# Kernel optimization log

Measured on AMD Instinct MI355X. Metric: run time of the kernel, lower is better.

The kernel has to match this reference:

```python
import jax, jax.numpy as jnp
import numpy as np


def _bag_mean(idx, table):
    # F.embedding_bag(mode='mean', padding_idx=last row): padding entries are
    # excluded from both the sum and the count. idx: [B, S, K]
    pad = table.shape[0] - 1
    mask = (idx != pad)[..., None].astype(table.dtype)          # [B,S,K,1]
    emb = table[idx] * mask                                      # [B,S,K,D]
    cnt = mask.sum(axis=-2)                                      # [B,S,1]
    s = emb.sum(axis=-2)                                         # [B,S,D]
    return jnp.where(cnt > 0, s / jnp.maximum(cnt, 1.0), 0.0)


def _subgraph_parts(qq, ques_table, skill_table, diff_table, area_table,
                    ques2skill, ques2diff, ques2area):
    qe = ques_table[qq]                                          # [B,S,D]
    sk = _bag_mean(ques2skill[qq], skill_table)                  # [B,S,D]
    df = diff_table[ques2diff[qq][..., 0]]                       # [B,S,D]
    ar = area_table[ques2area[qq][..., 0]]                       # [B,S,D]
    return qe, sk, df, ar


def reference(q, a, next_q, ques_table, skill_table, diff_table, area_table,
              ques2skill, ques2diff, ques2area, Wq, bq):
    # ---- get_subgraph_embedding (non-JunYi path) ----
    qe, sk, df, ar = _subgraph_parts(q, ques_table, skill_table, diff_table,
                                     area_table, ques2skill, ques2diff, ques2area)
    q_emb = (qe + sk + df + ar) / 4.0

    nqe, nsk, ndf, nar = _subgraph_parts(next_q, ques_table, skill_table,
                                         diff_table, area_table, ques2skill,
                                         ques2diff, ques2area)
    nq_emb = (nqe + nsk + ndf + nar) / 4.0
    # faithful to source: the averaging line for next_q is applied twice
    nq_emb = (nq_emb + nsk + ndf + nar) / 4.0

    q_emb = q_emb @ Wq.T + bq
    nq_emb = nq_emb @ Wq.T + bq

    # ---- Fusion_Module: answer==1 keeps first half, answer==0 keeps second ----
    af = a[..., None].astype(q_emb.dtype)                        # [B,S,1]
    input_emb = jnp.concatenate([q_emb * af, q_emb * (1.0 - af)], axis=-1)

    return jnp.concatenate([input_emb, nq_emb], axis=-1)        # [B,S,3D]


def setup_inputs() -> dict:
    key = jax.random.key(0)
    ks = jax.random.split(key, 12)
    B, S, D = 16, 2048, 128
    NQ, NS, ND, NA, K = 200001, 2001, 100, 50, 8
    return {
        "q": jax.random.randint(ks[0], (B, S), 0, NQ - 1),
        "a": jax.random.randint(ks[1], (B, S), 0, 2),
        "next_q": jax.random.randint(ks[2], (B, S), 0, NQ - 1),
        "ques_table": jax.random.normal(ks[3], (NQ, D), jnp.float32),
        "skill_table": jax.random.normal(ks[4], (NS, D), jnp.float32),
        "diff_table": jax.random.normal(ks[5], (ND, D), jnp.float32),
        "area_table": jax.random.normal(ks[6], (NA, D), jnp.float32),
        "ques2skill": jax.random.randint(ks[7], (NQ, K), 0, NS),
        "ques2diff": jax.random.randint(ks[8], (NQ, 1), 0, ND),
        "ques2area": jax.random.randint(ks[9], (NQ, 1), 0, NA),
        "Wq": jax.random.normal(ks[10], (D, D), jnp.float32) / np.sqrt(D),
        "bq": jax.random.normal(ks[11], (D,), jnp.float32) * 0.01,
    }
```

## Files before the change

### kernel.cpp

```cpp
#include <hip/hip_runtime.h>
#include <hip/hip_bf16.h>

typedef float  f32x4  __attribute__((ext_vector_type(4)));
typedef short  s16x8  __attribute__((ext_vector_type(8)));

#define PIN_LOADS() asm volatile("" ::: "memory")

__device__ __forceinline__ unsigned short f2bf(float f) {
    unsigned int u = __float_as_uint(f);
    unsigned int rnd = 0x7fffu + ((u >> 16) & 1u);
    return (unsigned short)((u + rnd) >> 16);
}

__device__ __forceinline__ void bf8_fma(const s16x8 v, float s, f32x4& a0, f32x4& a1) {
    const uint4 u = *(const uint4*)&v;
    a0[0] += s * __uint_as_float(u.x << 16);
    a0[1] += s * __uint_as_float(u.x & 0xffff0000u);
    a0[2] += s * __uint_as_float(u.y << 16);
    a0[3] += s * __uint_as_float(u.y & 0xffff0000u);
    a1[0] += s * __uint_as_float(u.z << 16);
    a1[1] += s * __uint_as_float(u.z & 0xffff0000u);
    a1[2] += s * __uint_as_float(u.w << 16);
    a1[3] += s * __uint_as_float(u.w & 0xffff0000u);
}

__global__ __launch_bounds__(256)
void h2kt_prep_wqb(const float* __restrict__ Wq, unsigned short* __restrict__ Wqb) {
    const int s  = blockIdx.x * 256 + threadIdx.x;
    const int f  = s >> 6, sl = s & 63;
    const int jt = f >> 2, kt = f & 3;
    const int row = jt * 16 + (sl & 15);
    const int col = kt * 32 + (sl >> 4) * 8;
    const float4 w0 = *(const float4*)(Wq + row * 128 + col);
    const float4 w1 = *(const float4*)(Wq + row * 128 + col + 4);
    s16x8 v;
    v[0] = (short)f2bf(w0.x); v[1] = (short)f2bf(w0.y);
    v[2] = (short)f2bf(w0.z); v[3] = (short)f2bf(w0.w);
    v[4] = (short)f2bf(w1.x); v[5] = (short)f2bf(w1.y);
    v[6] = (short)f2bf(w1.z); v[7] = (short)f2bf(w1.w);
    *(s16x8*)(Wqb + (size_t)s * 8) = v;
}

__global__ __launch_bounds__(64)
void h2kt_prep_tables(const float* __restrict__ skill, const float* __restrict__ diff,
                      const float* __restrict__ area, const unsigned short* __restrict__ Wqb,
                      unsigned short* __restrict__ T2)
{
    const int lane = threadIdx.x;
    const int cl = lane & 15, grp = lane >> 4;
    const int row16 = blockIdx.x * 16;

    int srow = row16 + cl;
    if (srow > 2150) srow = 2150;
    const float* src = (srow < 2001) ? skill + (size_t)srow * 128
                     : (srow < 2101) ? diff + (size_t)(srow - 2001) * 128
                                     : area + (size_t)(srow - 2101) * 128;
    s16x8 afr[4];
    #pragma unroll
    for (int kt = 0; kt < 4; ++kt) {
        const float4 v0 = *(const float4*)(src + kt * 32 + grp * 8);
        const float4 v1 = *(const float4*)(src + kt * 32 + grp * 8 + 4);
        s16x8 v;
        v[0] = (short)f2bf(v0.x); v[1] = (short)f2bf(v0.y);
        v[2] = (short)f2bf(v0.z); v[3] = (short)f2bf(v0.w);
        v[4] = (short)f2bf(v1.x); v[5] = (short)f2bf(v1.y);
        v[6] = (short)f2bf(v1.z); v[7] = (short)f2bf(v1.w);
        afr[kt] = v;
    }
    #pragma unroll
    for (int jt = 0; jt < 8; ++jt) {
        f32x4 acc = {0.f, 0.f, 0.f, 0.f};
        #pragma unroll
        for (int kt = 0; kt < 4; ++kt) {
            const s16x8 bf = *(const s16x8*)(Wqb + ((size_t)(jt * 4 + kt) * 64 + lane) * 8);
            acc = __builtin_amdgcn_mfma_f32_16x16x32_bf16(afr[kt], bf, acc, 0, 0, 0);
        }
        #pragma unroll
        for (int r = 0; r < 4; ++r) {
            const int orow = row16 + grp * 4 + r;
            if (orow < 2151) T2[(size_t)orow * 128 + jt * 16 + cl] = f2bf(acc[r]);
        }
    }
}

__global__ __launch_bounds__(128, 4)
void h2kt_fused(const int* __restrict__ q, const int* __restrict__ a_arr,
                const int* __restrict__ next_q,
                const float* __restrict__ ques_table,
                const int* __restrict__ q2s,
                const int* __restrict__ q2d,
                const int* __restrict__ q2a,
                const unsigned short* __restrict__ T2,
                const unsigned short* __restrict__ Wqb,
                const float* __restrict__ bq,
                float* __restrict__ out,
                int pad_idx)
{
    __shared__ __align__(16) unsigned char U[16 * 132 * 4];
    unsigned short* Q = (unsigned short*)U;
    float*          D = (float*)U;

    const int tid  = threadIdx.x;
    const int w    = tid >> 6;
    const int lane = tid & 63;
    const int cl   = lane & 15;
    const int grp  = lane >> 4;
    const int r0   = blockIdx.x * 16;
    const int base = r0 & 32767;
    const bool isnq = (r0 >= 32768);
    const int* __restrict__ QQ = isnq ? next_q : q;
    const float wq_ = isnq ? 0.0625f : 0.25f;
    const float wr_ = isnq ? 0.3125f : 0.25f;

    const int r2 = lane >> 5;
    const int c  = lane & 31;
    int qqv[4];
    #pragma unroll
    for (int p = 0; p < 4; ++p) qqv[p] = QQ[base + w * 8 + p * 2 + r2];

    const int row0 = w * 8 + grp;
    const int row1 = w * 8 + 4 + grp;
    const int qq20 = QQ[base + row0];
    const int qq21 = QQ[base + row1];
    int av0 = 1, av1 = 1;
    if (!isnq) { av0 = a_arr[base + row0]; av1 = a_arr[base + row1]; }

    f32x4 qv[4];
    #pragma unroll
    for (int p = 0; p < 4; ++p)
        qv[p] = *(const f32x4*)(ques_table + (size_t)qqv[p] * 128 + c * 4);

    const int4 A03 = *(const int4*)(q2s + (size_t)qq20 * 8);
    const int4 A47 = *(const int4*)(q2s + (size_t)qq20 * 8 + 4);
    const int4 B03 = *(const int4*)(q2s + (size_t)qq21 * 8);
    const int4 B47 = *(const int4*)(q2s + (size_t)qq21 * 8 + 4);
    const int di0 = q2d[qq20], ai0 = q2a[qq20];
    const int di1 = q2d[qq21], ai1 = q2a[qq21];
    const int sa[8] = {A03.x, A03.y, A03.z, A03.w, A47.x, A47.y, A47.z, A47.w};
    const int sb[8] = {B03.x, B03.y, B03.z, B03.w, B47.x, B47.y, B47.z, B47.w};

    s16x8 t0[10];
    #pragma unroll
    for (int i = 0; i < 8; ++i)
        t0[i] = *(const s16x8*)(T2 + (size_t)sa[i] * 128 + cl * 8);
    t0[8] = *(const s16x8*)(T2 + (size_t)(2001 + di0) * 128 + cl * 8);
    t0[9] = *(const s16x8*)(T2 + (size_t)(2101 + ai0) * 128 + cl * 8);
    PIN_LOADS();

    #pragma unroll
    for (int p = 0; p < 4; ++p) {
        ushort4 o;
        o.x = f2bf(wq_ * qv[p][0]); o.y = f2bf(wq_ * qv[p][1]);
        o.z = f2bf(wq_ * qv[p][2]); o.w = f2bf(wq_ * qv[p][3]);
        *(ushort4*)(Q + (size_t)(w * 8 + p * 2 + r2) * 136 + c * 4) = o;
    }

    s16x8 t1[10];
    #pragma unroll
    for (int i = 0; i < 8; ++i)
        t1[i] = *(const s16x8*)(T2 + (size_t)sb[i] * 128 + cl * 8);
    t1[8] = *(const s16x8*)(T2 + (size_t)(2001 + di1) * 128 + cl * 8);
    t1[9] = *(const s16x8*)(T2 + (size_t)(2101 + ai1) * 128 + cl * 8);
    PIN_LOADS();

    int cnt0 = 0, cnt1 = 0;
    #pragma unroll
    for (int i = 0; i < 8; ++i) { cnt0 += (sa[i] != pad_idx); cnt1 += (sb[i] != pad_idx); }
    const float cs0 = cnt0 > 0 ? wr_ / (float)cnt0 : 0.f;
    const float cs1 = cnt1 > 0 ? wr_ / (float)cnt1 : 0.f;

    f32x4 restA[2], restB[2];
    {
        f32x4 a0 = {0.f,0.f,0.f,0.f}, a1 = {0.f,0.f,0.f,0.f};
        #pragma unroll
        for (int i = 0; i < 8; ++i) bf8_fma(t0[i], (sa[i] != pad_idx) ? cs0 : 0.f, a0, a1);
        bf8_fma(t0[8], wr_, a0, a1);
        bf8_fma(t0[9], wr_, a0, a1);
        restA[0] = a0; restB[0] = a1;
    }
    {
        f32x4 a0 = {0.f,0.f,0.f,0.f}, a1 = {0.f,0.f,0.f,0.f};
        #pragma unroll
        for (int i = 0; i < 8; ++i) bf8_fma(t1[i], (sb[i] != pad_idx) ? cs1 : 0.f, a0, a1);
        bf8_fma(t1[8], wr_, a0, a1);
        bf8_fma(t1[9], wr_, a0, a1);
        restA[1] = a0; restB[1] = a1;
    }

    __syncthreads();

    s16x8 afr[4];
    #pragma unroll
    for (int kt = 0; kt < 4; ++kt)
        afr[kt] = *(const s16x8*)(Q + (size_t)cl * 136 + kt * 32 + grp * 8);

    __syncthreads();

    #pragma unroll
    for (int jt2 = 0; jt2 < 4; ++jt2) {
        const int jt = w * 4 + jt2;
        f32x4 acc = {0.f, 0.f, 0.f, 0.f};
        #pragma unroll
        for (int kt = 0; kt < 4; ++kt) {
            const s16x8 bf = *(const s16x8*)(Wqb + ((size_t)(jt * 4 + kt) * 64 + lane) * 8);
            acc = __builtin_amdgcn_mfma_f32_16x16x32_bf16(afr[kt], bf, acc, 0, 0, 0);
        }
        #pragma unroll
        for (int r = 0; r < 4; ++r)
            D[(size_t)(grp * 4 + r) * 132 + jt * 16 + cl] = acc[r];
    }

    __syncthreads();

    const f32x4 bq0 = *(const f32x4*)(bq + cl * 8);
    const f32x4 bq1 = *(const f32x4*)(bq + cl * 8 + 4);
    const f32x4 z = {0.f, 0.f, 0.f, 0.f};
    #pragma unroll
    for (int p = 0; p < 2; ++p) {
        const int row = w * 8 + p * 4 + grp;
        const f32x4 d0 = *(const f32x4*)(D + (size_t)row * 132 + cl * 8);
        const f32x4 d1 = *(const f32x4*)(D + (size_t)row * 132 + cl * 8 + 4);
        const f32x4 v0 = d0 + restA[p] + bq0;
        const f32x4 v1 = d1 + restB[p] + bq1;
        const size_t orow = (size_t)(base + row);
        const int avv = (p == 0) ? av0 : av1;
        if (!isnq) {
            const bool on = (avv != 0);
            *(f32x4*)(out + orow * 384 + cl * 8)           = on ? v0 : z;
            *(f32x4*)(out + orow * 384 + cl * 8 + 4)       = on ? v1 : z;
            *(f32x4*)(out + orow * 384 + 128 + cl * 8)     = on ? z : v0;
            *(f32x4*)(out + orow * 384 + 128 + cl * 8 + 4) = on ? z : v1;
        } else {
            *(f32x4*)(out + orow * 384 + 256 + cl * 8)     = v0;
            *(f32x4*)(out + orow * 384 + 256 + cl * 8 + 4) = v1;
        }
    }
}

extern "C" void kernel_launch(void* const* d_in, const int* in_sizes, int n_in,
                              void* d_out, int out_size, void* d_ws, size_t ws_size,
                              hipStream_t stream) {
    const int*   q          = (const int*)d_in[0];
    const int*   a          = (const int*)d_in[1];
    const int*   next_q     = (const int*)d_in[2];
    const float* ques_table = (const float*)d_in[3];
    const float* skill_tab  = (const float*)d_in[4];
    const float* diff_tab   = (const float*)d_in[5];
    const float* area_tab   = (const float*)d_in[6];
    const int*   q2s        = (const int*)d_in[7];
    const int*   q2d        = (const int*)d_in[8];
    const int*   q2a        = (const int*)d_in[9];
    const float* Wq         = (const float*)d_in[10];
    const float* bq         = (const float*)d_in[11];
    float* out = (float*)d_out;

    const int NS = in_sizes[4] / 128;
    const int pad_idx = NS - 1;

    unsigned short* Wqb = (unsigned short*)d_ws;
    unsigned short* T2  = Wqb + (size_t)2048 * 8;

    h2kt_prep_wqb<<<8, 256, 0, stream>>>(Wq, Wqb);
    h2kt_prep_tables<<<135, 64, 0, stream>>>(skill_tab, diff_tab, area_tab, Wqb, T2);
    h2kt_fused<<<4096, 128, 0, stream>>>(q, a, next_q, ques_table,
                                         q2s, q2d, q2a, T2, Wqb, bq, out, pad_idx);
}
```

Baseline: 44.78 us.

## Merge prep kernels and precompute per-row gather descriptors before fused kernel

The two prep kernels become one launch. Blocks in that launch now do three jobs: convert Wq to bf16, project the skill/diff/area tables (reading Wq directly instead of waiting on Wqb), and build a 48-byte descriptor per row holding the question id, skill ids, diff/area row offsets and the answer bit. The fused kernel then reads these descriptors instead of chasing q -> q2s/q2d/q2a itself. This removes one launch and a dependent gather stage from the main kernel. In exchange it adds about 3 MB of descriptor writes and reads through the workspace.

```diff
diff --git a/kernel.cpp b/kernel.cpp
--- a/kernel.cpp
+++ b/kernel.cpp
@@ -25,71 +25,98 @@
 }
 
 __global__ __launch_bounds__(256)
-void h2kt_prep_wqb(const float* __restrict__ Wq, unsigned short* __restrict__ Wqb) {
-    const int s  = blockIdx.x * 256 + threadIdx.x;
-    const int f  = s >> 6, sl = s & 63;
-    const int jt = f >> 2, kt = f & 3;
-    const int row = jt * 16 + (sl & 15);
-    const int col = kt * 32 + (sl >> 4) * 8;
-    const float4 w0 = *(const float4*)(Wq + row * 128 + col);
-    const float4 w1 = *(const float4*)(Wq + row * 128 + col + 4);
-    s16x8 v;
-    v[0] = (short)f2bf(w0.x); v[1] = (short)f2bf(w0.y);
-    v[2] = (short)f2bf(w0.z); v[3] = (short)f2bf(w0.w);
-    v[4] = (short)f2bf(w1.x); v[5] = (short)f2bf(w1.y);
-    v[6] = (short)f2bf(w1.z); v[7] = (short)f2bf(w1.w);
-    *(s16x8*)(Wqb + (size_t)s * 8) = v;
-}
-
-__global__ __launch_bounds__(64)
-void h2kt_prep_tables(const float* __restrict__ skill, const float* __restrict__ diff,
-                      const float* __restrict__ area, const unsigned short* __restrict__ Wqb,
-                      unsigned short* __restrict__ T2)
+void h2kt_prep(const float* __restrict__ Wq,
+               const float* __restrict__ skill, const float* __restrict__ diff,
+               const float* __restrict__ area,
+               const int* __restrict__ q, const int* __restrict__ next_q,
+               const int* __restrict__ a_arr,
+               const int* __restrict__ q2s, const int* __restrict__ q2d,
+               const int* __restrict__ q2a,
+               unsigned short* __restrict__ Wqb,
+               unsigned short* __restrict__ T2,
+               int* __restrict__ desc,
+               int pad_idx)
 {
-    const int lane = threadIdx.x;
-    const int cl = lane & 15, grp = lane >> 4;
-    const int row16 = blockIdx.x * 16;
-
-    int srow = row16 + cl;
-    if (srow > 2150) srow = 2150;
-    const float* src = (srow < 2001) ? skill + (size_t)srow * 128
-                     : (srow < 2101) ? diff + (size_t)(srow - 2001) * 128
-                                     : area + (size_t)(srow - 2101) * 128;
-    s16x8 afr[4];
-    #pragma unroll
-    for (int kt = 0; kt < 4; ++kt) {
-        const float4 v0 = *(const float4*)(src + kt * 32 + grp * 8);
-        const float4 v1 = *(const float4*)(src + kt * 32 + grp * 8 + 4);
+    const int bid = blockIdx.x, tid = threadIdx.x;
+
+    if (bid < 8) {
+        const int s  = bid * 256 + tid;
+        const int f  = s >> 6, sl = s & 63;
+        const int jt = f >> 2, kt = f & 3;
+        const int row = jt * 16 + (sl & 15);
+        const int col = kt * 32 + (sl >> 4) * 8;
+        const float4 w0 = *(const float4*)(Wq + row * 128 + col);
+        const float4 w1 = *(const float4*)(Wq + row * 128 + col + 4);
         s16x8 v;
-        v[0] = (short)f2bf(v0.x); v[1] = (short)f2bf(v0.y);
-        v[2] = (short)f2bf(v0.z); v[3] = (short)f2bf(v0.w);
-        v[4] = (short)f2bf(v1.x); v[5] = (short)f2bf(v1.y);
-        v[6] = (short)f2bf(v1.z); v[7] = (short)f2bf(v1.w);
-        afr[kt] = v;
-    }
-    #pragma unroll
-    for (int jt = 0; jt < 8; ++jt) {
-        f32x4 acc = {0.f, 0.f, 0.f, 0.f};
+        v[0] = (short)f2bf(w0.x); v[1] = (short)f2bf(w0.y);
+        v[2] = (short)f2bf(w0.z); v[3] = (short)f2bf(w0.w);
+        v[4] = (short)f2bf(w1.x); v[5] = (short)f2bf(w1.y);
+        v[6] = (short)f2bf(w1.z); v[7] = (short)f2bf(w1.w);
+        *(s16x8*)(Wqb + (size_t)s * 8) = v;
+    } else if (bid < 42) {
+        const int lane = tid & 63;
+        const int cl = lane & 15, grp = lane >> 4;
+        const int row16 = ((bid - 8) * 4 + (tid >> 6)) * 16;
+        if (row16 > 2150) return;
+
+        int srow = row16 + cl;
+        if (srow > 2150) srow = 2150;
+        const float* src = (srow < 2001) ? skill + (size_t)srow * 128
+                         : (srow < 2101) ? diff + (size_t)(srow - 2001) * 128
+                                         : area + (size_t)(srow - 2101) * 128;
+        s16x8 afr[4];
         #pragma unroll
         for (int kt = 0; kt < 4; ++kt) {
-            const s16x8 bf = *(const s16x8*)(Wqb + ((size_t)(jt * 4 + kt) * 64 + lane) * 8);
-            acc = __builtin_amdgcn_mfma_f32_16x16x32_bf16(afr[kt], bf, acc, 0, 0, 0);
-        }
-        #pragma unroll
-        for (int r = 0; r < 4; ++r) {
-            const int orow = row16 + grp * 4 + r;
-            if (orow < 2151) T2[(size_t)orow * 128 + jt * 16 + cl] = f2bf(acc[r]);
-        }
+            const float4 v0 = *(const float4*)(src + kt * 32 + grp * 8);
+            const float4 v1 = *(const float4*)(src + kt * 32 + grp * 8 + 4);
+            s16x8 v;
+            v[0] = (short)f2bf(v0.x); v[1] = (short)f2bf(v0.y);
+            v[2] = (short)f2bf(v0.z); v[3] = (short)f2bf(v0.w);
+            v[4] = (short)f2bf(v1.x); v[5] = (short)f2bf(v1.y);
+            v[6] = (short)f2bf(v1.z); v[7] = (short)f2bf(v1.w);
+            afr[kt] = v;
+        }
+        #pragma unroll
+        for (int jt = 0; jt < 8; ++jt) {
+            f32x4 acc = {0.f, 0.f, 0.f, 0.f};
+            #pragma unroll
+            for (int kt = 0; kt < 4; ++kt) {
+                const float* wp = Wq + (jt * 16 + cl) * 128 + kt * 32 + grp * 8;
+                const float4 w0 = *(const float4*)(wp);
+                const float4 w1 = *(const float4*)(wp + 4);
+                s16x8 bf;
+                bf[0] = (short)f2bf(w0.x); bf[1] = (short)f2bf(w0.y);
+                bf[2] = (short)f2bf(w0.z); bf[3] = (short)f2bf(w0.w);
+                bf[4] = (short)f2bf(w1.x); bf[5] = (short)f2bf(w1.y);
+                bf[6] = (short)f2bf(w1.z); bf[7] = (short)f2bf(w1.w);
+                acc = __builtin_amdgcn_mfma_f32_16x16x32_bf16(afr[kt], bf, acc, 0, 0, 0);
+            }
+            #pragma unroll
+            for (int r = 0; r < 4; ++r) {
+                const int orow = row16 + grp * 4 + r;
+                if (orow < 2151) T2[(size_t)orow * 128 + jt * 16 + cl] = f2bf(acc[r]);
+            }
+        }
+    } else {
+        const int g = (bid - 42) * 256 + tid;
+        const int p = g & 32767;
+        const bool isnq = (g >= 32768);
+        const int qq = isnq ? next_q[p] : q[p];
+        const int4 s03 = *(const int4*)(q2s + (size_t)qq * 8);
+        const int4 s47 = *(const int4*)(q2s + (size_t)qq * 8 + 4);
+        const int di = q2d[qq];
+        const int ai = q2a[qq];
+        const int av = isnq ? 1 : a_arr[p];
+        int4* d = (int4*)(desc + (size_t)g * 12);
+        d[0] = make_int4(qq, s03.x, s03.y, s03.z);
+        d[1] = make_int4(s03.w, s47.x, s47.y, s47.z);
+        d[2] = make_int4(s47.w, 2001 + di, 2101 + ai, av);
     }
 }
 
 __global__ __launch_bounds__(128, 4)
-void h2kt_fused(const int* __restrict__ q, const int* __restrict__ a_arr,
-                const int* __restrict__ next_q,
+void h2kt_fused(const int* __restrict__ desc,
                 const float* __restrict__ ques_table,
-                const int* __restrict__ q2s,
-                const int* __restrict__ q2d,
-                const int* __restrict__ q2a,
                 const unsigned short* __restrict__ T2,
                 const unsigned short* __restrict__ Wqb,
                 const float* __restrict__ bq,
@@ -105,10 +132,9 @@
     const int lane = tid & 63;
     const int cl   = lane & 15;
     const int grp  = lane >> 4;
-    const int r0   = blockIdx.x * 16;
-    const int base = r0 & 32767;
-    const bool isnq = (r0 >= 32768);
-    const int* __restrict__ QQ = isnq ? next_q : q;
+    const int g0   = blockIdx.x * 16;
+    const int base = g0 & 32767;
+    const bool isnq = (g0 >= 32768);
     const float wq_ = isnq ? 0.0625f : 0.25f;
     const float wr_ = isnq ? 0.3125f : 0.25f;
 
@@ -116,35 +142,29 @@
     const int c  = lane & 31;
     int qqv[4];
     #pragma unroll
-    for (int p = 0; p < 4; ++p) qqv[p] = QQ[base + w * 8 + p * 2 + r2];
-
-    const int row0 = w * 8 + grp;
-    const int row1 = w * 8 + 4 + grp;
-    const int qq20 = QQ[base + row0];
-    const int qq21 = QQ[base + row1];
-    int av0 = 1, av1 = 1;
-    if (!isnq) { av0 = a_arr[base + row0]; av1 = a_arr[base + row1]; }
+    for (int p = 0; p < 4; ++p)
+        qqv[p] = desc[(size_t)(g0 + w * 8 + p * 2 + r2) * 12];
+
+    const int4* D0 = (const int4*)(desc + (size_t)(g0 + w * 8 + grp) * 12);
+    const int4* D1 = (const int4*)(desc + (size_t)(g0 + w * 8 + 4 + grp) * 12);
+    const int4 a0i = D0[0], a1i = D0[1], a2i = D0[2];
+    const int4 b0i = D1[0], b1i = D1[1], b2i = D1[2];
 
     f32x4 qv[4];
     #pragma unroll
     for (int p = 0; p < 4; ++p)
         qv[p] = *(const f32x4*)(ques_table + (size_t)qqv[p] * 128 + c * 4);
 
-    const int4 A03 = *(const int4*)(q2s + (size_t)qq20 * 8);
-    const int4 A47 = *(const int4*)(q2s + (size_t)qq20 * 8 + 4);
-    const int4 B03 = *(const int4*)(q2s + (size_t)qq21 * 8);
-    const int4 B47 = *(const int4*)(q2s + (size_t)qq21 * 8 + 4);
-    const int di0 = q2d[qq20], ai0 = q2a[qq20];
-    const int di1 = q2d[qq21], ai1 = q2a[qq21];
-    const int sa[8] = {A03.x, A03.y, A03.z, A03.w, A47.x, A47.y, A47.z, A47.w};
-    const int sb[8] = {B03.x, B03.y, B03.z, B03.w, B47.x, B47.y, B47.z, B47.w};
+    const int sa[8] = {a0i.y, a0i.z, a0i.w, a1i.x, a1i.y, a1i.z, a1i.w, a2i.x};
+    const int sb[8] = {b0i.y, b0i.z, b0i.w, b1i.x, b1i.y, b1i.z, b1i.w, b2i.x};
+    const int av0 = a2i.w, av1 = b2i.w;
 
     s16x8 t0[10];
     #pragma unroll
     for (int i = 0; i < 8; ++i)
         t0[i] = *(const s16x8*)(T2 + (size_t)sa[i] * 128 + cl * 8);
-    t0[8] = *(const s16x8*)(T2 + (size_t)(2001 + di0) * 128 + cl * 8);
-    t0[9] = *(const s16x8*)(T2 + (size_t)(2101 + ai0) * 128 + cl * 8);
+    t0[8] = *(const s16x8*)(T2 + (size_t)a2i.y * 128 + cl * 8);
+    t0[9] = *(const s16x8*)(T2 + (size_t)a2i.z * 128 + cl * 8);
     PIN_LOADS();
 
     #pragma unroll
@@ -159,8 +179,8 @@
     #pragma unroll
     for (int i = 0; i < 8; ++i)
         t1[i] = *(const s16x8*)(T2 + (size_t)sb[i] * 128 + cl * 8);
-    t1[8] = *(const s16x8*)(T2 + (size_t)(2001 + di1) * 128 + cl * 8);
-    t1[9] = *(const s16x8*)(T2 + (size_t)(2101 + ai1) * 128 + cl * 8);
+    t1[8] = *(const s16x8*)(T2 + (size_t)b2i.y * 128 + cl * 8);
+    t1[9] = *(const s16x8*)(T2 + (size_t)b2i.z * 128 + cl * 8);
     PIN_LOADS();
 
     int cnt0 = 0, cnt1 = 0;
@@ -257,11 +277,12 @@
     const int NS = in_sizes[4] / 128;
     const int pad_idx = NS - 1;
 
-    unsigned short* Wqb = (unsigned short*)d_ws;
-    unsigned short* T2  = Wqb + (size_t)2048 * 8;
-
-    h2kt_prep_wqb<<<8, 256, 0, stream>>>(Wq, Wqb);
-    h2kt_prep_tables<<<135, 64, 0, stream>>>(skill_tab, diff_tab, area_tab, Wqb, T2);
-    h2kt_fused<<<4096, 128, 0, stream>>>(q, a, next_q, ques_table,
-                                         q2s, q2d, q2a, T2, Wqb, bq, out, pad_idx);
-}
+    int*            descp = (int*)d_ws;
+    unsigned short* Wqb   = (unsigned short*)((char*)d_ws + (size_t)65536 * 48);
+    unsigned short* T2    = Wqb + (size_t)2048 * 8;
+
+    h2kt_prep<<<298, 256, 0, stream>>>(Wq, skill_tab, diff_tab, area_tab,
+                                       q, next_q, a, q2s, q2d, q2a,
+                                       Wqb, T2, descp, pad_idx);
+    h2kt_fused<<<4096, 128, 0, stream>>>(descp, ques_table, T2, Wqb, bq, out, pad_idx);
+}
```

Measured after the change: 42.91 us. -4.2%, faster.
